# Kernel tuning notes

Measured on AMD Instinct MI355X. Metric: run time of the kernel, lower is better.

## Reference

```python
import jax, jax.numpy as jnp
import numpy as np

N_HEAD = 16
EPS = 1e-06


def setup_inputs() -> dict:
    key = jax.random.key(0)
    ks = jax.random.split(key, 9)
    B, S, Q, D, Dp = 16, 4096, 49, 1024, 1024
    INIT = 0.02  # GPT-2 style init scale keeps exp(scores) finite
    x = jax.random.normal(ks[0], (B, S, D), dtype=jnp.float32)
    y = jax.random.normal(ks[1], (B, Q, Dp), dtype=jnp.float32)
    # multiplicative binary mask applied to exp(scores), shaped [1,1,49,S//64,64]
    attention_mask = (jax.random.uniform(ks[2], (1, 1, Q, S // 64, 64)) > 0.5).astype(jnp.float32)
    W_attn = jax.random.normal(ks[3], (D, 2 * D), dtype=jnp.float32) * INIT
    b_attn = jnp.zeros((2 * D,), dtype=jnp.float32)
    W_mlp = jax.random.normal(ks[4], (Dp, D), dtype=jnp.float32) * INIT
    b_mlp = jnp.zeros((D,), dtype=jnp.float32)
    W_proj = jax.random.normal(ks[5], (D, Dp), dtype=jnp.float32) * INIT
    b_proj = jnp.zeros((Dp,), dtype=jnp.float32)
    return {"x": x, "y": y, "attention_mask": attention_mask,
            "W_attn": W_attn, "b_attn": b_attn, "W_mlp": W_mlp, "b_mlp": b_mlp,
            "W_proj": W_proj, "b_proj": b_proj}


def reference(x, y, attention_mask, W_attn, b_attn, W_mlp, b_mlp, W_proj, b_proj):
    B, S, D = x.shape
    Q = y.shape[1]
    H = N_HEAD
    hd = D // H
    # c_attn (Conv1D): x @ W + b -> split into key, value
    kv = x @ W_attn + b_attn                       # [B,S,2D]
    key, value = kv[..., :D], kv[..., D:]
    k = key.reshape(B, S, H, hd).transpose(0, 2, 3, 1)    # [B,H,hd,S] (k=True perm)
    v = value.reshape(B, S, H, hd).transpose(0, 2, 1, 3)  # [B,H,S,hd]
    q = (y @ W_mlp + b_mlp).reshape(B, Q, H, hd).transpose(0, 2, 1, 3)  # [B,H,Q,hd]
    # fp32 scores, scaled by sqrt(head_dim)
    w = jnp.einsum('bhqd,bhds->bhqs', q.astype(jnp.float32), k.astype(jnp.float32))
    w = w / jnp.sqrt(jnp.float32(hd))
    # custom exp + multiplicative blocked mask + epsilon-stabilized normalize
    e = (jnp.exp(w).reshape(B, H, 49, -1, 64) * attention_mask).reshape(B, H, Q, S)
    w = e / (e.sum(-1, keepdims=True) + EPS)
    # PV matmul, cast to bf16 as in the original, then merge heads
    a = jnp.einsum('bhqs,bhsd->bhqd', w, v.astype(jnp.float32)).astype(jnp.bfloat16)
    a = a.transpose(0, 2, 1, 3).reshape(B, Q, D).astype(jnp.float32)
    out = a @ W_proj + b_proj                      # c_proj
    return out
```

## Files before the change

kernel.cpp:

```cpp
#include <hip/hip_runtime.h>
#include <cstdint>

typedef __bf16 bf16x8 __attribute__((ext_vector_type(8)));
typedef float f32x4 __attribute__((ext_vector_type(4)));
typedef unsigned short u16;

#define GBAR() asm volatile("s_barrier" ::: "memory")
#define SBAR0() __builtin_amdgcn_sched_barrier(0)
#define LGKM0() do { asm volatile("s_waitcnt lgkmcnt(0)" ::: "memory"); SBAR0(); } while (0)
#define LGKM4() do { asm volatile("s_waitcnt lgkmcnt(4)" ::: "memory"); SBAR0(); } while (0)
#define VM6()  asm volatile("s_waitcnt vmcnt(6)" ::: "memory")
#define VM8()  asm volatile("s_waitcnt vmcnt(8)" ::: "memory")
#define MFMA16(a, b, c) __builtin_amdgcn_mfma_f32_16x16x32_bf16((a), (b), (c), 0, 0, 0)

__device__ __forceinline__ u16 f2bf(float f) {
  unsigned u = __builtin_bit_cast(unsigned, f);
  u += 0x7fffu + ((u >> 16) & 1u);
  return (u16)(u >> 16);
}
__device__ __forceinline__ float bfu(ushort4 v, int r) {
  unsigned short s = (r == 0) ? v.x : (r == 1) ? v.y : (r == 2) ? v.z : v.w;
  return __builtin_bit_cast(float, (unsigned)s << 16);
}

__global__ void cast_f32_bf16(const float* __restrict__ in, u16* __restrict__ out,
                              int n4in, int n4out) {
  int i = blockIdx.x * blockDim.x + threadIdx.x;
  int stride = gridDim.x * blockDim.x;
  for (; i < n4out; i += stride) {
    ushort4 o;
    if (i < n4in) {
      float4 v = ((const float4*)in)[i];
      o.x = f2bf(v.x); o.y = f2bf(v.y); o.z = f2bf(v.z); o.w = f2bf(v.w);
    } else {
      o.x = 0; o.y = 0; o.z = 0; o.w = 0;
    }
    ((ushort4*)out)[i] = o;
  }
}

__global__ void transpose_cast(const float* __restrict__ in, u16* __restrict__ out,
                               int R, int C) {
  __shared__ float t[64][65];
  int tc = blockIdx.x * 64, tr = blockIdx.y * 64;
  int c = threadIdx.x & 63, r0 = threadIdx.x >> 6;
  #pragma unroll
  for (int p = 0; p < 16; ++p) {
    int r = p * 4 + r0;
    t[r][c] = in[(long)(tr + r) * C + (tc + c)];
  }
  __syncthreads();
  #pragma unroll
  for (int p = 0; p < 16; ++p) {
    int r = p * 4 + r0;
    out[(long)(tc + r) * R + (tr + c)] = f2bf(t[c][r]);
  }
}

__global__ void mask_prep(const float* __restrict__ in, u16* __restrict__ out) {
  __shared__ float t[64][65];
  int s0 = blockIdx.x * 64;
  int c = threadIdx.x & 63, r0 = threadIdx.x >> 6;
  #pragma unroll
  for (int p = 0; p < 16; ++p) {
    int q = p * 4 + r0;
    t[q][c] = (q < 49) ? in[(long)q * 4096 + s0 + c] : 0.f;
  }
  __syncthreads();
  #pragma unroll
  for (int p = 0; p < 16; ++p) {
    int r = p * 4 + r0;
    out[(long)(s0 + r) * 64 + c] = f2bf(t[c][r]);
  }
}

template<int MODE>
__global__ __launch_bounds__(512, 2) void gemm256(
    const u16* __restrict__ A, const u16* __restrict__ BT,
    const float* __restrict__ bias, void* __restrict__ outp)
{
  __shared__ __align__(16) char lds[131072];

  int tid = threadIdx.x;
  int l = tid & 63, w = tid >> 6;
  int wr = w >> 2, wc = w & 3;
  int lr = l & 15, lh = l >> 4;

  int bid = blockIdx.x;
  int mt, nt;
  long out_off = 0;
  const u16* Ap = A;
  const u16* BTp = BT;
  if constexpr (MODE == 0) {
    int wg = (bid & 7) * 128 + (bid >> 3);
    mt = wg >> 2; nt = wg & 3;
  } else {
    int wg = (bid & 7) * 8 + (bid >> 3);
    mt = wg & 3; nt = wg >> 2;
    int b = blockIdx.y;
    BTp = BT + (long)b * 4194304;
    out_off = (long)b * 4194304;
  }
  long Arow0 = (long)mt * 256;
  long Brow0 = (long)nt * 256;

  int rho = (w << 3) + (l >> 3);
  int csw = ((l & 7) ^ (l >> 3)) << 3;
  const u16* agA = Ap + (Arow0 + rho) * 1024 + csw;
  int browoff = (w >> 2) * 64 + (w & 3) * 8 + (l >> 3);
  const u16* agB = BTp + (Brow0 + browoff) * 1024 + csw;
  char* ldsAthr = lds + rho * 128 + (l & 7) * 16;
  char* ldsBthr = lds + 32768 + browoff * 128 + (l & 7) * 16;

  auto SA = [&](int dt, int st, int mh) {
    char* d = ldsAthr + (dt & 1) * 65536 + mh * 8192;
    const u16* s = agA + (long)st * 64 + mh * 65536;
    __builtin_amdgcn_global_load_lds(
        (const __attribute__((address_space(1))) void*)s,
        (__attribute__((address_space(3))) void*)d, 16, 0, 0);
    __builtin_amdgcn_global_load_lds(
        (const __attribute__((address_space(1))) void*)(s + 131072),
        (__attribute__((address_space(3))) void*)(d + 16384), 16, 0, 0);
  };
  auto SB = [&](int dt, int st, int h) {
    char* d = ldsBthr + (dt & 1) * 65536 + h * 4096;
    const u16* s = agB + (long)st * 64 + h * 32768;
    __builtin_amdgcn_global_load_lds(
        (const __attribute__((address_space(1))) void*)s,
        (__attribute__((address_space(3))) void*)d, 16, 0, 0);
    __builtin_amdgcn_global_load_lds(
        (const __attribute__((address_space(1))) void*)(s + 131072),
        (__attribute__((address_space(3))) void*)(d + 16384), 16, 0, 0);
  };

  int arow_b = (wr * 128 + lr) * 128;
  int brow_b = (wc * 64 + lr) * 128 + 32768;
  int xr0 = (lh ^ (lr & 7)) << 4;
  int xr1 = ((4 + lh) ^ (lr & 7)) << 4;

  f32x4 acc[8][4];
  #pragma unroll
  for (int m = 0; m < 8; ++m)
    #pragma unroll
    for (int n = 0; n < 4; ++n) acc[m][n] = f32x4{0.f, 0.f, 0.f, 0.f};

  bf16x8 af[4][2], bn0[2][2], bn1[2][2];

  SA(0, 0, 0); SB(0, 0, 0); SB(0, 0, 1); SA(0, 0, 1);
  SA(1, 1, 0); SB(1, 1, 0); SB(1, 1, 1);
  VM6();
  GBAR();

  for (int t = 0; t < 16; ++t) {
    int buf = (t & 1) << 16;
    #pragma unroll
    for (int m = 0; m < 4; ++m) {
      af[m][0] = *(const bf16x8*)(lds + buf + arow_b + m * 2048 + xr0);
      af[m][1] = *(const bf16x8*)(lds + buf + arow_b + m * 2048 + xr1);
    }
    #pragma unroll
    for (int n = 0; n < 2; ++n) {
      bn0[n][0] = *(const bf16x8*)(lds + buf + brow_b + n * 2048 + xr0);
      bn0[n][1] = *(const bf16x8*)(lds + buf + brow_b + n * 2048 + xr1);
    }
    SBAR0();
    #pragma unroll
    for (int n = 0; n < 2; ++n) {
      bn1[n][0] = *(const bf16x8*)(lds + buf + brow_b + 4096 + n * 2048 + xr0);
      bn1[n][1] = *(const bf16x8*)(lds + buf + brow_b + 4096 + n * 2048 + xr1);
    }
    SBAR0();
    { int tt = t + 1; SA(tt, tt < 16 ? tt : 15, 1); }
    LGKM4();
    __builtin_amdgcn_s_setprio(1);
    #pragma unroll
    for (int m = 0; m < 4; ++m)
      #pragma unroll
      for (int n = 0; n < 2; ++n) {
        acc[m][n] = MFMA16(af[m][0], bn0[n][0], acc[m][n]);
        acc[m][n] = MFMA16(af[m][1], bn0[n][1], acc[m][n]);
      }
    __builtin_amdgcn_s_setprio(0);
    GBAR();
    { int tt = t + 2; SA(tt, tt < 16 ? tt : 15, 0); }
    LGKM0();
    __builtin_amdgcn_s_setprio(1);
    #pragma unroll
    for (int m = 0; m < 4; ++m)
      #pragma unroll
      for (int n = 0; n < 2; ++n) {
        acc[m][2 + n] = MFMA16(af[m][0], bn1[n][0], acc[m][2 + n]);
        acc[m][2 + n] = MFMA16(af[m][1], bn1[n][1], acc[m][2 + n]);
      }
    __builtin_amdgcn_s_setprio(0);
    #pragma unroll
    for (int m = 0; m < 4; ++m) {
      af[m][0] = *(const bf16x8*)(lds + buf + arow_b + 8192 + m * 2048 + xr0);
      af[m][1] = *(const bf16x8*)(lds + buf + arow_b + 8192 + m * 2048 + xr1);
    }
    GBAR();
    { int tt = t + 2; SB(tt, tt < 16 ? tt : 15, 0); }
    LGKM0();
    __builtin_amdgcn_s_setprio(1);
    #pragma unroll
    for (int m = 0; m < 4; ++m)
      #pragma unroll
      for (int n = 0; n < 2; ++n) {
        acc[4 + m][n] = MFMA16(af[m][0], bn0[n][0], acc[4 + m][n]);
        acc[4 + m][n] = MFMA16(af[m][1], bn0[n][1], acc[4 + m][n]);
      }
    __builtin_amdgcn_s_setprio(0);
    { int tt = t + 2; SB(tt, tt < 16 ? tt : 15, 1); }
    __builtin_amdgcn_s_setprio(1);
    #pragma unroll
    for (int m = 0; m < 4; ++m)
      #pragma unroll
      for (int n = 0; n < 2; ++n) {
        acc[4 + m][2 + n] = MFMA16(af[m][0], bn1[n][0], acc[4 + m][2 + n]);
        acc[4 + m][2 + n] = MFMA16(af[m][1], bn1[n][1], acc[4 + m][2 + n]);
      }
    __builtin_amdgcn_s_setprio(0);
    VM6();
    GBAR();
  }

  asm volatile("s_waitcnt vmcnt(0)" ::: "memory");

  #pragma unroll
  for (int m = 0; m < 8; ++m) {
    #pragma unroll
    for (int n = 0; n < 4; ++n) {
      #pragma unroll
      for (int r = 0; r < 4; ++r) {
        long row = Arow0 + wr * 128 + m * 16 + lh * 4 + r;
        long col = Brow0 + wc * 64 + n * 16 + lr;
        float v = acc[m][n][r];
        if constexpr (MODE == 0) {
          v += bias[col];
          long addr = (row >> 12) * 4194304 + (col >> 6) * 262144
                    + (row & 4095) * 64 + (col & 63);
          ((u16*)outp)[addr] = f2bf(v);
        } else {
          v += bias[1024 + row];
          ((u16*)outp)[out_off + row * 4096 + col] = f2bf(v);
        }
      }
    }
  }
}

template<int MODE>
__global__ __launch_bounds__(256, 2) void gemm_bt(
    const u16* __restrict__ A, const u16* __restrict__ BT,
    const float* __restrict__ bias, void* __restrict__ outp)
{
  __shared__ u16 As[128][64];
  __shared__ u16 Bs[128][64];

  int bid = blockIdx.x;
  int mt = bid >> 3, nt = bid & 7;

  int tid = threadIdx.x;
  int l = tid & 63, w = tid >> 6;
  int wr = w >> 1, wc = w & 1;
  int lr = l & 15, lh = l >> 4;

  f32x4 acc[4][4];
  #pragma unroll
  for (int i = 0; i < 4; ++i)
    #pragma unroll
    for (int j = 0; j < 4; ++j)
      acc[i][j] = f32x4{0.f, 0.f, 0.f, 0.f};

  long arow0 = (long)mt * 128;
  long brow0 = (long)nt * 128;
  int srow = w * 8 + (l >> 3);
  int scol = (l & 7) * 8;
  const u16* ag = A + (arow0 + srow) * 1024 + scol;
  const u16* bg = BT + (brow0 + srow) * 1024 + scol;
  u16* asl = &As[srow][scol];
  u16* bsl = &Bs[srow][scol];

  for (int kt = 0; kt < 16; ++kt) {
    int ko = kt * 64;
    #pragma unroll
    for (int p = 0; p < 4; ++p)
      __builtin_amdgcn_global_load_lds(
          (const __attribute__((address_space(1))) void*)(ag + (long)p * 32 * 1024 + ko),
          (__attribute__((address_space(3))) void*)(asl + p * 32 * 64), 16, 0, 0);
    #pragma unroll
    for (int p = 0; p < 4; ++p)
      __builtin_amdgcn_global_load_lds(
          (const __attribute__((address_space(1))) void*)(bg + (long)p * 32 * 1024 + ko),
          (__attribute__((address_space(3))) void*)(bsl + p * 32 * 64), 16, 0, 0);
    __syncthreads();
    #pragma unroll
    for (int kk = 0; kk < 2; ++kk) {
      bf16x8 af[4], bfr[4];
      #pragma unroll
      for (int m = 0; m < 4; ++m)
        af[m] = *(const bf16x8*)&As[wr * 64 + m * 16 + lr][kk * 32 + lh * 8];
      #pragma unroll
      for (int n = 0; n < 4; ++n)
        bfr[n] = *(const bf16x8*)&Bs[wc * 64 + n * 16 + lr][kk * 32 + lh * 8];
      #pragma unroll
      for (int m = 0; m < 4; ++m)
        #pragma unroll
        for (int n = 0; n < 4; ++n)
          acc[m][n] = MFMA16(af[m], bfr[n], acc[m][n]);
    }
    __syncthreads();
  }

  #pragma unroll
  for (int m = 0; m < 4; ++m) {
    #pragma unroll
    for (int n = 0; n < 4; ++n) {
      #pragma unroll
      for (int r = 0; r < 4; ++r) {
        int row = (int)arow0 + wr * 64 + m * 16 + lh * 4 + r;
        int col = (int)brow0 + wc * 64 + n * 16 + lr;
        float v = acc[m][n][r];
        if constexpr (MODE == 2) {
          if (row < 784) {
            v += bias[col];
            int b = row / 49, qi = row - b * 49;
            long addr = ((long)(b * 16 + (col >> 6)) * 64 + qi) * 64 + (col & 63);
            ((u16*)outp)[addr] = f2bf(v);
          }
        } else {
          if (row < 784) {
            v += bias[col];
            ((float*)outp)[(long)row * 1024 + col] = v;
          }
        }
      }
    }
  }
}

__global__ __launch_bounds__(256, 4) void attn_part(
    const u16* __restrict__ Kt, const u16* __restrict__ Vt, const u16* __restrict__ Q,
    const u16* __restrict__ maskT,
    float* __restrict__ partA, float* __restrict__ prs)
{
  __shared__ __align__(16) char lds[40960];

  int bh = blockIdx.x, chunk = blockIdx.y;
  int tid = threadIdx.x;
  int l = tid & 63, w = tid >> 6;
  int lr = l & 15, lh = l >> 4;

  const u16* Kb = Kt + (long)bh * 262144;
  const u16* Vb = Vt + (long)bh * 262144;
  const u16* Qb = Q + (long)bh * 4096;

  int t0 = chunk * 21 + (chunk > 0 ? 1 : 0);
  int nt = 21 + (chunk == 0 ? 1 : 0);
  int tmax = t0 + nt - 1;

  int strow = tid >> 3;
  int sc = tid & 7;

  auto STAGE = [&](int buf, int tt) {
    long s0 = (long)tt * 64;
    #pragma unroll
    for (int h = 0; h < 2; ++h) {
      int row = h * 32 + strow;
      int cs = (sc ^ (row & 7)) << 3;
      const u16* ksrc = Kb + (s0 + row) * 64 + cs;
      char* kdst = lds + buf * 8192 + row * 128 + sc * 16;
      __builtin_amdgcn_global_load_lds(
          (const __attribute__((address_space(1))) void*)ksrc,
          (__attribute__((address_space(3))) void*)kdst, 16, 0, 0);
      const u16* vsrc = Vb + (long)row * 4096 + s0 + cs;
      char* vdst = lds + 16384 + buf * 8192 + row * 128 + sc * 16;
      __builtin_amdgcn_global_load_lds(
          (const __attribute__((address_space(1))) void*)vsrc,
          (__attribute__((address_space(3))) void*)vdst, 16, 0, 0);
    }
  };

  bf16x8 qf[2];
  #pragma unroll
  for (int kf2 = 0; kf2 < 2; ++kf2)
    qf[kf2] = *(const bf16x8*)(Qb + (w * 16 + lr) * 64 + kf2 * 32 + lh * 8);

  bf16x8 ones;
  #pragma unroll
  for (int j = 0; j < 8; ++j) ones[j] = (__bf16)1.0f;

  f32x4 acc_a[4];
  #pragma unroll
  for (int n = 0; n < 4; ++n) acc_a[n] = f32x4{0.f, 0.f, 0.f, 0.f};
  f32x4 acc_rs = f32x4{0.f, 0.f, 0.f, 0.f};

  char* Pw = lds + 32768 + w * 2048;
  const u16* mbase = maskT + w * 16 + lh * 4;

  STAGE(0, t0);
  STAGE(1, t0 + 1);
  ushort4 mvu[4];
  #pragma unroll
  for (int sf = 0; sf < 4; ++sf)
    mvu[sf] = *(const ushort4*)(mbase + ((long)t0 * 64 + sf * 16 + lr) * 64);
  VM8();
  GBAR();

  for (int it = 0; it < nt; ++it) {
    int buf = it & 1;
    const char* Kl = lds + buf * 8192;
    const char* Vl = lds + 16384 + buf * 8192;

    int tn = it + 1 < nt ? t0 + it + 1 : tmax;
    ushort4 mvn[4];
    #pragma unroll
    for (int sf = 0; sf < 4; ++sf)
      mvn[sf] = *(const ushort4*)(mbase + ((long)tn * 64 + sf * 16 + lr) * 64);

    bf16x8 kf[4][2];
    #pragma unroll
    for (int sf = 0; sf < 4; ++sf) {
      int srw = sf * 16 + lr;
      int xb = srw & 7;
      kf[sf][0] = *(const bf16x8*)(Kl + srw * 128 + ((lh ^ xb) << 4));
      kf[sf][1] = *(const bf16x8*)(Kl + srw * 128 + (((4 + lh) ^ xb) << 4));
    }
    f32x4 lg[4];
    #pragma unroll
    for (int sf = 0; sf < 4; ++sf) {
      f32x4 t = f32x4{0.f, 0.f, 0.f, 0.f};
      t = MFMA16(qf[0], kf[sf][0], t);
      t = MFMA16(qf[1], kf[sf][1], t);
      lg[sf] = t;
    }

    bf16x8 vf[2][4];
    #pragma unroll
    for (int k2 = 0; k2 < 2; ++k2)
      #pragma unroll
      for (int n = 0; n < 4; ++n) {
        int vrow = n * 16 + lr;
        vf[k2][n] = *(const bf16x8*)(Vl + vrow * 128 + (((k2 * 4 + lh) ^ (lr & 7)) << 4));
      }

    #pragma unroll
    for (int sf = 0; sf < 4; ++sf) {
      #pragma unroll
      for (int r = 0; r < 4; ++r) {
        int qq = lh * 4 + r;
        float e = __expf(lg[sf][r] * 0.125f) * bfu(mvu[sf], r);
        int byte = (qq * 128 + (sf * 16 + lr) * 2) ^ ((qq & 7) << 4);
        *(u16*)(Pw + byte) = f2bf(e);
      }
    }

    #pragma unroll
    for (int k2 = 0; k2 < 2; ++k2) {
      int byte = (lr * 128 + k2 * 64 + lh * 16) ^ ((lr & 7) << 4);
      bf16x8 pf;
      __builtin_memcpy(&pf, Pw + byte, 16);
      #pragma unroll
      for (int n = 0; n < 4; ++n)
        acc_a[n] = MFMA16(pf, vf[k2][n], acc_a[n]);
      acc_rs = MFMA16(pf, ones, acc_rs);
    }

    LGKM0();
    GBAR();
    { int tt = it + 2 < nt ? t0 + it + 2 : tmax; STAGE(buf, tt); }
    VM8();
    GBAR();

    #pragma unroll
    for (int sf = 0; sf < 4; ++sf) mvu[sf] = mvn[sf];
  }

  long base = ((long)bh * 3 + chunk) * 64;
  #pragma unroll
  for (int r = 0; r < 4; ++r) {
    int q = w * 16 + lh * 4 + r;
    if (lr == 0) prs[base + q] = acc_rs[r];
    #pragma unroll
    for (int n = 0; n < 4; ++n)
      partA[(base + q) * 64 + n * 16 + lr] = acc_a[n][r];
  }
}

__global__ __launch_bounds__(256) void attn_reduce(
    const float* __restrict__ partA, const float* __restrict__ prs,
    u16* __restrict__ Abf)
{
  int bh = blockIdx.x;
  int t = threadIdx.x;
  int q = t >> 2, d0 = (t & 3) * 16;
  if (q >= 49) return;
  int b = bh >> 4, h = bh & 15;

  float rs = 1e-6f;
  #pragma unroll
  for (int c = 0; c < 3; ++c) rs += prs[((long)bh * 3 + c) * 64 + q];

  #pragma unroll
  for (int j = 0; j < 4; ++j) {
    float4 s = float4{0.f, 0.f, 0.f, 0.f};
    #pragma unroll
    for (int c = 0; c < 3; ++c) {
      float4 v = *(const float4*)(partA + (((long)bh * 3 + c) * 64 + q) * 64 + d0 + j * 4);
      s.x += v.x; s.y += v.y; s.z += v.z; s.w += v.w;
    }
    ushort4 o;
    o.x = f2bf(s.x / rs); o.y = f2bf(s.y / rs);
    o.z = f2bf(s.z / rs); o.w = f2bf(s.w / rs);
    *(ushort4*)(Abf + ((long)(b * 49 + q) * 1024 + h * 64 + d0 + j * 4)) = o;
  }
}

extern "C" void kernel_launch(void* const* d_in, const int* in_sizes, int n_in,
                              void* d_out, int out_size, void* d_ws, size_t ws_size,
                              hipStream_t stream) {
  const float* x      = (const float*)d_in[0];
  const float* y      = (const float*)d_in[1];
  const float* mask   = (const float*)d_in[2];
  const float* W_attn = (const float*)d_in[3];
  const float* b_attn = (const float*)d_in[4];
  const float* W_mlp  = (const float*)d_in[5];
  const float* b_mlp  = (const float*)d_in[6];
  const float* W_proj = (const float*)d_in[7];
  const float* b_proj = (const float*)d_in[8];

  if (ws_size < 417333248ULL) return;

  char* ws = (char*)d_ws;
  u16* x_bf    = (u16*)(ws);
  u16* Kt      = (u16*)(ws + 134217728L);
  u16* Vt      = (u16*)(ws + 268435456L);
  u16* WT_attn = (u16*)(ws + 402653184L);
  u16* WT_mlp  = (u16*)(ws + 406847488L);
  u16* WT_proj = (u16*)(ws + 408944640L);
  u16* y_bf    = (u16*)(ws + 411041792L);
  u16* q_ws    = (u16*)(ws + 412876800L);
  u16* a_bf    = (u16*)(ws + 414973952L);
  u16* maskT   = (u16*)(ws + 416808960L);
  float* partA = (float*)(ws);
  float* prs   = (float*)(ws + 16777216L);

  cast_f32_bf16<<<2048, 256, 0, stream>>>(x, x_bf, 16777216, 16777216);
  cast_f32_bf16<<<896, 256, 0, stream>>>(y, y_bf, 200704, 229376);
  transpose_cast<<<dim3(32, 16), 256, 0, stream>>>(W_attn, WT_attn, 1024, 2048);
  transpose_cast<<<dim3(16, 16), 256, 0, stream>>>(W_mlp, WT_mlp, 1024, 1024);
  transpose_cast<<<dim3(16, 16), 256, 0, stream>>>(W_proj, WT_proj, 1024, 1024);
  mask_prep<<<64, 256, 0, stream>>>(mask, maskT);

  gemm256<0><<<1024, 512, 0, stream>>>(x_bf, WT_attn, b_attn, Kt);
  gemm256<1><<<dim3(64, 16), 512, 0, stream>>>(WT_attn + 1048576, x_bf, b_attn, Vt);
  gemm_bt<2><<<56, 256, 0, stream>>>(y_bf, WT_mlp, b_mlp, q_ws);

  attn_part<<<dim3(256, 3), 256, 0, stream>>>(Kt, Vt, q_ws, maskT, partA, prs);
  attn_reduce<<<256, 256, 0, stream>>>(partA, prs, a_bf);

  gemm_bt<3><<<56, 256, 0, stream>>>(a_bf, WT_proj, b_proj, d_out);
}
```

Measured before the change: 498.1 us.

## Restructure GEMM main loop into unrolled two-tile ping-pong schedule

Unrolls the GEMM K-loop by two so each LDS buffer offset is a compile-time constant. It reorders global-to-LDS prefetches and LDS fragment reads around the four MFMA quadrants, using more barriers and full lgkmcnt waits. The goal is to interleave loads with MFMA work more evenly across waves. The extra s_barrier calls and stricter waits may add stalls, and the reordered prefetch slots must not overwrite buffers that are still being read.

Result: no change. 493.0 us (-1.0%).

```diff
diff --git a/kernel.cpp b/kernel.cpp
--- a/kernel.cpp
+++ b/kernel.cpp
@@ -8,7 +8,6 @@
 #define GBAR() asm volatile("s_barrier" ::: "memory")
 #define SBAR0() __builtin_amdgcn_sched_barrier(0)
 #define LGKM0() do { asm volatile("s_waitcnt lgkmcnt(0)" ::: "memory"); SBAR0(); } while (0)
-#define LGKM4() do { asm volatile("s_waitcnt lgkmcnt(4)" ::: "memory"); SBAR0(); } while (0)
 #define VM6()  asm volatile("s_waitcnt vmcnt(6)" ::: "memory")
 #define VM8()  asm volatile("s_waitcnt vmcnt(8)" ::: "memory")
 #define MFMA16(a, b, c) __builtin_amdgcn_mfma_f32_16x16x32_bf16((a), (b), (c), 0, 0, 0)
@@ -146,81 +145,89 @@
 
   bf16x8 af[4][2], bn0[2][2], bn1[2][2];
 
-  SA(0, 0, 0); SB(0, 0, 0); SB(0, 0, 1); SA(0, 0, 1);
-  SA(1, 1, 0); SB(1, 1, 0); SB(1, 1, 1);
-  VM6();
-  GBAR();
-
-  for (int t = 0; t < 16; ++t) {
-    int buf = (t & 1) << 16;
+  auto RD_AF0 = [&](int buf) {
     #pragma unroll
     for (int m = 0; m < 4; ++m) {
       af[m][0] = *(const bf16x8*)(lds + buf + arow_b + m * 2048 + xr0);
       af[m][1] = *(const bf16x8*)(lds + buf + arow_b + m * 2048 + xr1);
     }
+  };
+  auto RD_AF1 = [&](int buf) {
+    #pragma unroll
+    for (int m = 0; m < 4; ++m) {
+      af[m][0] = *(const bf16x8*)(lds + buf + arow_b + 8192 + m * 2048 + xr0);
+      af[m][1] = *(const bf16x8*)(lds + buf + arow_b + 8192 + m * 2048 + xr1);
+    }
+  };
+  auto RD_BN0 = [&](int buf) {
     #pragma unroll
     for (int n = 0; n < 2; ++n) {
       bn0[n][0] = *(const bf16x8*)(lds + buf + brow_b + n * 2048 + xr0);
       bn0[n][1] = *(const bf16x8*)(lds + buf + brow_b + n * 2048 + xr1);
     }
-    SBAR0();
+  };
+  auto RD_BN1 = [&](int buf) {
     #pragma unroll
     for (int n = 0; n < 2; ++n) {
       bn1[n][0] = *(const bf16x8*)(lds + buf + brow_b + 4096 + n * 2048 + xr0);
       bn1[n][1] = *(const bf16x8*)(lds + buf + brow_b + 4096 + n * 2048 + xr1);
     }
-    SBAR0();
-    { int tt = t + 1; SA(tt, tt < 16 ? tt : 15, 1); }
-    LGKM4();
+  };
+  auto Q = [&](int mo, int no, bf16x8 (&bn)[2][2]) {
     __builtin_amdgcn_s_setprio(1);
     #pragma unroll
     for (int m = 0; m < 4; ++m)
       #pragma unroll
       for (int n = 0; n < 2; ++n) {
-        acc[m][n] = MFMA16(af[m][0], bn0[n][0], acc[m][n]);
-        acc[m][n] = MFMA16(af[m][1], bn0[n][1], acc[m][n]);
+        acc[mo + m][no + n] = MFMA16(af[m][0], bn[n][0], acc[mo + m][no + n]);
+        acc[mo + m][no + n] = MFMA16(af[m][1], bn[n][1], acc[mo + m][no + n]);
       }
     __builtin_amdgcn_s_setprio(0);
-    GBAR();
+  };
+
+  SA(0, 0, 0); SA(0, 0, 1); SB(0, 0, 0); SB(0, 0, 1);
+  SA(1, 1, 0); SA(1, 1, 1); SB(1, 1, 0);
+  VM6(); GBAR();
+
+  for (int i = 0; i < 8; ++i) {
+    int t = 2 * i;
+    RD_AF0(0); RD_BN0(0); SBAR0();
+    SB(t + 1, t + 1, 1);
+    GBAR(); LGKM0();
+    Q(0, 0, bn0);
+    GBAR();
+    RD_BN1(0); SBAR0();
     { int tt = t + 2; SA(tt, tt < 16 ? tt : 15, 0); }
-    LGKM0();
-    __builtin_amdgcn_s_setprio(1);
-    #pragma unroll
-    for (int m = 0; m < 4; ++m)
-      #pragma unroll
-      for (int n = 0; n < 2; ++n) {
-        acc[m][2 + n] = MFMA16(af[m][0], bn1[n][0], acc[m][2 + n]);
-        acc[m][2 + n] = MFMA16(af[m][1], bn1[n][1], acc[m][2 + n]);
-      }
-    __builtin_amdgcn_s_setprio(0);
-    #pragma unroll
-    for (int m = 0; m < 4; ++m) {
-      af[m][0] = *(const bf16x8*)(lds + buf + arow_b + 8192 + m * 2048 + xr0);
-      af[m][1] = *(const bf16x8*)(lds + buf + arow_b + 8192 + m * 2048 + xr1);
-    }
-    GBAR();
+    GBAR(); LGKM0();
+    Q(0, 2, bn1);
+    GBAR();
+    RD_AF1(0); SBAR0();
     { int tt = t + 2; SB(tt, tt < 16 ? tt : 15, 0); }
-    LGKM0();
-    __builtin_amdgcn_s_setprio(1);
-    #pragma unroll
-    for (int m = 0; m < 4; ++m)
-      #pragma unroll
-      for (int n = 0; n < 2; ++n) {
-        acc[4 + m][n] = MFMA16(af[m][0], bn0[n][0], acc[4 + m][n]);
-        acc[4 + m][n] = MFMA16(af[m][1], bn0[n][1], acc[4 + m][n]);
-      }
-    __builtin_amdgcn_s_setprio(0);
+    GBAR(); LGKM0();
+    Q(4, 0, bn0);
+    GBAR();
+    { int tt = t + 2; SA(tt, tt < 16 ? tt : 15, 1); }
+    GBAR(); VM6();
+    Q(4, 2, bn1);
+    GBAR();
+    RD_AF0(65536); RD_BN0(65536); SBAR0();
     { int tt = t + 2; SB(tt, tt < 16 ? tt : 15, 1); }
-    __builtin_amdgcn_s_setprio(1);
-    #pragma unroll
-    for (int m = 0; m < 4; ++m)
-      #pragma unroll
-      for (int n = 0; n < 2; ++n) {
-        acc[4 + m][2 + n] = MFMA16(af[m][0], bn1[n][0], acc[4 + m][2 + n]);
-        acc[4 + m][2 + n] = MFMA16(af[m][1], bn1[n][1], acc[4 + m][2 + n]);
-      }
-    __builtin_amdgcn_s_setprio(0);
-    VM6();
+    GBAR(); LGKM0();
+    Q(0, 0, bn0);
+    GBAR();
+    RD_BN1(65536); SBAR0();
+    { int tt = t + 3; SA(tt, tt < 16 ? tt : 15, 0); }
+    GBAR(); LGKM0();
+    Q(0, 2, bn1);
+    GBAR();
+    RD_AF1(65536); SBAR0();
+    { int tt = t + 3; SB(tt, tt < 16 ? tt : 15, 0); }
+    GBAR(); LGKM0();
+    Q(4, 0, bn0);
+    GBAR();
+    { int tt = t + 3; SA(tt, tt < 16 ? tt : 15, 1); }
+    GBAR(); VM6();
+    Q(4, 2, bn1);
     GBAR();
   }
 
```
